# Optimization experiments

Measured on AMD Instinct MI355X. Metric: run time of the kernel, lower is better.

The kernel has to match this reference:

```python
import jax, jax.numpy as jnp
import numpy as np

N_NODES = 50000
N_EDGES = 800000
HIDDEN = 128
EDGE_DIM = 16
N_HEADS = 8
HEAD_DIM = HIDDEN // N_HEADS
SCALE = 1.0 / np.sqrt(HEAD_DIM).astype(np.float32)
LN_EPS = 1e-5


def setup_inputs() -> dict:
    key = jax.random.key(0)
    ks = jax.random.split(key, 24)
    s = 0.02

    def w(k, shape):
        return jax.random.normal(k, shape, dtype=jnp.float32) * s

    inp = {
        "node_features": jax.random.normal(ks[0], (N_NODES, HIDDEN), dtype=jnp.float32),
        "edge_index": jax.random.randint(ks[1], (2, N_EDGES), 0, N_NODES, dtype=jnp.int32),
        "edge_features": jax.random.normal(ks[2], (N_EDGES, EDGE_DIM), dtype=jnp.float32),
        # projections stored as [in, out] (y = x @ W + b)
        "Wq": w(ks[3], (HIDDEN, HIDDEN)), "bq": jnp.zeros((HIDDEN,), jnp.float32),
        "Wk": w(ks[4], (HIDDEN, HIDDEN)), "bk": jnp.zeros((HIDDEN,), jnp.float32),
        "Wv": w(ks[5], (HIDDEN, HIDDEN)), "bv": jnp.zeros((HIDDEN,), jnp.float32),
        "Wb1": w(ks[6], (EDGE_DIM, N_HEADS)), "bb1": jnp.zeros((N_HEADS,), jnp.float32),
        "Wb2": w(ks[7], (N_HEADS, N_HEADS)), "bb2": jnp.zeros((N_HEADS,), jnp.float32),
        "Wo": w(ks[8], (HIDDEN, HIDDEN)), "bo": jnp.zeros((HIDDEN,), jnp.float32),
        "Wf1": w(ks[9], (HIDDEN, 2 * HIDDEN)), "bf1": jnp.zeros((2 * HIDDEN,), jnp.float32),
        "Wf2": w(ks[10], (2 * HIDDEN, HIDDEN)), "bf2": jnp.zeros((HIDDEN,), jnp.float32),
        "g1": jnp.ones((HIDDEN,), jnp.float32), "be1": jnp.zeros((HIDDEN,), jnp.float32),
        "g2": jnp.ones((HIDDEN,), jnp.float32), "be2": jnp.zeros((HIDDEN,), jnp.float32),
    }
    return inp


def _layer_norm(x, gamma, beta):
    mu = jnp.mean(x, axis=-1, keepdims=True)
    var = jnp.mean(jnp.square(x - mu), axis=-1, keepdims=True)
    return (x - mu) * jax.lax.rsqrt(var + LN_EPS) * gamma + beta


def reference(node_features, edge_index, edge_features,
              Wq, bq, Wk, bk, Wv, bv, Wb1, bb1, Wb2, bb2,
              Wo, bo, Wf1, bf1, Wf2, bf2, g1, be1, g2, be2):
    n_nodes = node_features.shape[0]
    src, dst = edge_index[0], edge_index[1]

    q = (node_features @ Wq + bq).reshape(n_nodes, N_HEADS, HEAD_DIM)
    k = (node_features @ Wk + bk).reshape(n_nodes, N_HEADS, HEAD_DIM)
    v = (node_features @ Wv + bv).reshape(n_nodes, N_HEADS, HEAD_DIM)

    # per-edge attention logits [E, H]
    edge_bias = jax.nn.silu(edge_features @ Wb1 + bb1) @ Wb2 + bb2
    logits = jnp.sum(q[dst] * k[src], axis=-1) * SCALE + edge_bias

    # segment softmax over edges sharing the same dst node
    max_s = jax.ops.segment_max(logits, dst, num_segments=n_nodes)
    exp_s = jnp.exp(logits - max_s[dst])
    norm = jax.ops.segment_sum(exp_s, dst, num_segments=n_nodes)
    attn = exp_s / jnp.clip(norm[dst], 1e-12)

    # weighted aggregation [N, H, D] -> [N, hidden]
    weighted = attn[:, :, None] * v[src]
    aggregated = jax.ops.segment_sum(weighted, dst, num_segments=n_nodes)
    aggregated = aggregated.reshape(n_nodes, HIDDEN)

    x = _layer_norm(node_features + (aggregated @ Wo + bo), g1, be1)
    ffn = jax.nn.silu(x @ Wf1 + bf1) @ Wf2 + bf2
    return _layer_norm(x + ffn, g2, be2)
```

## Files before the change

kernel.cpp:

```cpp
#include <hip/hip_runtime.h>
#include <hip/hip_bf16.h>
#include <math.h>

#define HIDDEN 128
#define EDGE_DIM 16
#define N_HEADS 8
#define QK_SCALE 0.25f
#define LN_EPS 1e-5f

using bf16x8 = __attribute__((ext_vector_type(8))) short;
using f32x4 = __attribute__((ext_vector_type(4))) float;
using f32x4v = __attribute__((ext_vector_type(4))) float;
using f32x2 = __attribute__((ext_vector_type(2))) float;
using i32x4 = __attribute__((ext_vector_type(4))) int;
typedef __hip_bfloat16 bf16;

__device__ __forceinline__ float b2f(short u) {
  union { unsigned int i; float f; } c;
  c.i = ((unsigned int)(unsigned short)u) << 16;
  return c.f;
}
__device__ __forceinline__ short f2b(float f) {
  bf16 h = __float2bfloat16(f);
  union { bf16 b; short s; } c;
  c.b = h;
  return c.s;
}
__device__ __forceinline__ unsigned char f2fp8(float f) {
  int pk = __builtin_amdgcn_cvt_pk_fp8_f32(f, f, 0, false);
  return (unsigned char)(pk & 0xff);
}

__global__ __launch_bounds__(256) void conv_weights_kernel(
    const float* __restrict__ Wq, const float* __restrict__ Wk, const float* __restrict__ Wv,
    const float* __restrict__ bq, const float* __restrict__ bk, const float* __restrict__ bv,
    const float* __restrict__ Wo, const float* __restrict__ Wf1, const float* __restrict__ Wf2,
    bf16* __restrict__ Wqkv_t, bf16* __restrict__ Wo_t, bf16* __restrict__ Wf1_t,
    bf16* __restrict__ Wf2_t, float* __restrict__ bqkv) {
  int i = blockIdx.x * 256 + threadIdx.x;
  if (i < 49152) {
    int n = i >> 7, k = i & 127;
    const float* W = (n < 128) ? Wq : ((n < 256) ? Wk : Wv);
    int nn = n & 127;
    Wqkv_t[i] = __float2bfloat16(W[k * 128 + nn]);
  } else if (i < 65536) {
    int j = i - 49152;
    int n = j >> 7, k = j & 127;
    Wo_t[j] = __float2bfloat16(Wo[k * 128 + n]);
  } else if (i < 98304) {
    int j = i - 65536;
    int n = j >> 7, k = j & 127;
    Wf1_t[j] = __float2bfloat16(Wf1[k * 256 + n]);
  } else if (i < 131072) {
    int j = i - 98304;
    int n = j >> 8, k = j & 255;
    Wf2_t[j] = __float2bfloat16(Wf2[k * 128 + n]);
  }
  if (i < 384) bqkv[i] = (i < 128) ? bq[i] : ((i < 256) ? bk[i - 128] : bv[i - 256]);
}

template <int K, int EPI, int OUTBF, int AF32>
__global__ __launch_bounds__(256) void mfma_gemm_kernel(
    const void* __restrict__ Ap, const bf16* __restrict__ Wt,
    const float* __restrict__ bias, void* __restrict__ Cout, int M, int Nc) {
  const int tid = threadIdx.x;
  const int w = tid >> 6, l = tid & 63;
  const int wr = w >> 1, wc = w & 1;
  const int lr = l & 15, lk = l >> 4;
  const int bm = blockIdx.y * 64;
  const int bn = blockIdx.x * 128 + wc * 64;

  f32x4 acc[2][4] = {};
  const int arow0 = bm + wr * 32 + lr;

  for (int k0 = 0; k0 < K; k0 += 128) {
    bf16x8 bfr[4][4];
#pragma unroll
    for (int fn = 0; fn < 4; ++fn) {
      const bf16* wp = Wt + (size_t)(bn + fn * 16 + lr) * K + k0 + lk * 8;
#pragma unroll
      for (int ks = 0; ks < 4; ++ks) bfr[fn][ks] = *(const bf16x8*)(wp + ks * 32);
    }
    bf16x8 afr[2][4];
#pragma unroll
    for (int fr = 0; fr < 2; ++fr) {
      int row = arow0 + fr * 16;
      if (row >= M) row = M - 1;
      if (AF32) {
        const float* ap = (const float*)Ap + (size_t)row * K + k0 + lk * 8;
#pragma unroll
        for (int ks = 0; ks < 4; ++ks) {
          float4 x = *(const float4*)(ap + ks * 32);
          float4 y = *(const float4*)(ap + ks * 32 + 4);
          bf16x8 t;
          t[0] = f2b(x.x); t[1] = f2b(x.y); t[2] = f2b(x.z); t[3] = f2b(x.w);
          t[4] = f2b(y.x); t[5] = f2b(y.y); t[6] = f2b(y.z); t[7] = f2b(y.w);
          afr[fr][ks] = t;
        }
      } else {
        const bf16* ap = (const bf16*)Ap + (size_t)row * K + k0 + lk * 8;
#pragma unroll
        for (int ks = 0; ks < 4; ++ks) afr[fr][ks] = *(const bf16x8*)(ap + ks * 32);
      }
    }
#pragma unroll
    for (int ks = 0; ks < 4; ++ks)
#pragma unroll
      for (int fr = 0; fr < 2; ++fr)
#pragma unroll
        for (int fn = 0; fn < 4; ++fn)
          acc[fr][fn] = __builtin_amdgcn_mfma_f32_16x16x32_bf16(afr[fr][ks], bfr[fn][ks],
                                                                acc[fr][fn], 0, 0, 0);
  }

#pragma unroll
  for (int fn = 0; fn < 4; ++fn) {
    const int col = bn + fn * 16 + lr;
    const float bv = bias[col];
#pragma unroll
    for (int fr = 0; fr < 2; ++fr) {
      const int rbase = bm + wr * 32 + fr * 16 + lk * 4;
#pragma unroll
      for (int r = 0; r < 4; ++r) {
        int row = rbase + r;
        if (row < M) {
          float o = acc[fr][fn][r] + bv;
          if (EPI == 1) o = o / (1.f + __expf(-o));
          if (OUTBF)
            ((bf16*)Cout)[(size_t)row * Nc + col] = __float2bfloat16(o);
          else
            ((float*)Cout)[(size_t)row * Nc + col] = o;
        }
      }
    }
  }
}

__global__ __launch_bounds__(256) void mfma_gemm_qkv_kernel(
    const float* __restrict__ A, const bf16* __restrict__ Wt,
    const float* __restrict__ bias, bf16* __restrict__ qb,
    unsigned char* __restrict__ kv8, int M) {
  __shared__ __align__(16) char lds[64 * 272];
  const int tid = threadIdx.x;
  const int w = tid >> 6, l = tid & 63;
  const int wr = w >> 1, wc = w & 1;
  const int lr = l & 15, lk = l >> 4;
  const int bm = blockIdx.y * 64;
  const int bn = blockIdx.x * 128 + wc * 64;

  f32x4 acc[2][4] = {};
  const int arow0 = bm + wr * 32 + lr;

  {
    bf16x8 bfr[4][4];
#pragma unroll
    for (int fn = 0; fn < 4; ++fn) {
      const bf16* wp = Wt + (size_t)(bn + fn * 16 + lr) * 128 + lk * 8;
#pragma unroll
      for (int ks = 0; ks < 4; ++ks) bfr[fn][ks] = *(const bf16x8*)(wp + ks * 32);
    }
    bf16x8 afr[2][4];
#pragma unroll
    for (int fr = 0; fr < 2; ++fr) {
      int row = arow0 + fr * 16;
      if (row >= M) row = M - 1;
      const float* ap = A + (size_t)row * 128 + lk * 8;
#pragma unroll
      for (int ks = 0; ks < 4; ++ks) {
        float4 x = *(const float4*)(ap + ks * 32);
        float4 y = *(const float4*)(ap + ks * 32 + 4);
        bf16x8 t;
        t[0] = f2b(x.x); t[1] = f2b(x.y); t[2] = f2b(x.z); t[3] = f2b(x.w);
        t[4] = f2b(y.x); t[5] = f2b(y.y); t[6] = f2b(y.z); t[7] = f2b(y.w);
        afr[fr][ks] = t;
      }
    }
#pragma unroll
    for (int ks = 0; ks < 4; ++ks)
#pragma unroll
      for (int fr = 0; fr < 2; ++fr)
#pragma unroll
        for (int fn = 0; fn < 4; ++fn)
          acc[fr][fn] = __builtin_amdgcn_mfma_f32_16x16x32_bf16(afr[fr][ks], bfr[fn][ks],
                                                                acc[fr][fn], 0, 0, 0);
  }

  const bool isQ = (blockIdx.x == 0);
  if (isQ) {
    short* sq = (short*)lds;
#pragma unroll
    for (int fn = 0; fn < 4; ++fn) {
      const int col = wc * 64 + fn * 16 + lr;
      const float bv = bias[bn + fn * 16 + lr];
#pragma unroll
      for (int fr = 0; fr < 2; ++fr) {
#pragma unroll
        for (int r = 0; r < 4; ++r) {
          int rl = wr * 32 + fr * 16 + lk * 4 + r;
          sq[rl * 136 + col] = f2b(acc[fr][fn][r] + bv);
        }
      }
    }
  } else {
    unsigned char* s8 = (unsigned char*)lds;
#pragma unroll
    for (int fn = 0; fn < 4; ++fn) {
      const int col = wc * 64 + fn * 16 + lr;
      const float bv = bias[bn + fn * 16 + lr];
#pragma unroll
      for (int fr = 0; fr < 2; ++fr) {
#pragma unroll
        for (int r = 0; r < 4; ++r) {
          int rl = wr * 32 + fr * 16 + lk * 4 + r;
          s8[rl * 144 + col] = f2fp8(acc[fr][fn][r] + bv);
        }
      }
    }
  }
  __syncthreads();

  const int row = tid >> 2, seg = tid & 3;
  const int grow = bm + row;
  if (grow < M) {
    if (isQ) {
      const int4* src = (const int4*)(lds + row * 272 + seg * 64);
      int4* dst = (int4*)(qb + (size_t)grow * 128 + seg * 32);
      dst[0] = src[0];
      dst[1] = src[1];
      dst[2] = src[2];
      dst[3] = src[3];
    } else {
      const int4* src = (const int4*)(lds + row * 144 + seg * 32);
      int4* dst = (int4*)(kv8 + (size_t)grow * 256 + (blockIdx.x == 1 ? 0 : 128) + seg * 32);
      dst[0] = src[0];
      dst[1] = src[1];
    }
  }
}

template <int K>
__global__ __launch_bounds__(256) void mfma_gemm_ln_kernel(
    const bf16* __restrict__ A, const bf16* __restrict__ Wt,
    const float* __restrict__ bias, const float* __restrict__ R,
    const float* __restrict__ gam, const float* __restrict__ bet,
    float* __restrict__ y, bf16* __restrict__ yb, int M) {
  const int tid = threadIdx.x;
  const int w = tid >> 6, l = tid & 63;
  const int wr = w >> 1, wc = w & 1;
  const int lr = l & 15, lk = l >> 4;
  const int bm = blockIdx.x * 64;
  const int bn = wc * 64;

  f32x4 acc[2][4] = {};
  const int arow0 = bm + wr * 32 + lr;

  for (int k0 = 0; k0 < K; k0 += 128) {
    bf16x8 bfr[4][4];
#pragma unroll
    for (int fn = 0; fn < 4; ++fn) {
      const bf16* wp = Wt + (size_t)(bn + fn * 16 + lr) * K + k0 + lk * 8;
#pragma unroll
      for (int ks = 0; ks < 4; ++ks) bfr[fn][ks] = *(const bf16x8*)(wp + ks * 32);
    }
    bf16x8 afr[2][4];
#pragma unroll
    for (int fr = 0; fr < 2; ++fr) {
      int row = arow0 + fr * 16;
      if (row >= M) row = M - 1;
      const bf16* ap = A + (size_t)row * K + k0 + lk * 8;
#pragma unroll
      for (int ks = 0; ks < 4; ++ks) afr[fr][ks] = *(const bf16x8*)(ap + ks * 32);
    }
#pragma unroll
    for (int ks = 0; ks < 4; ++ks)
#pragma unroll
      for (int fr = 0; fr < 2; ++fr)
#pragma unroll
        for (int fn = 0; fn < 4; ++fn)
          acc[fr][fn] = __builtin_amdgcn_mfma_f32_16x16x32_bf16(afr[fr][ks], bfr[fn][ks],
                                                                acc[fr][fn], 0, 0, 0);
  }

  float bv[4], gv[4], ev[4];
#pragma unroll
  for (int fn = 0; fn < 4; ++fn) {
    int col = bn + fn * 16 + lr;
    bv[fn] = bias[col];
    gv[fn] = gam[col];
    ev[fn] = bet[col];
  }
  float ps[2][4], psq[2][4];
#pragma unroll
  for (int fr = 0; fr < 2; ++fr) {
#pragma unroll
    for (int r = 0; r < 4; ++r) {
      int row = bm + wr * 32 + fr * 16 + lk * 4 + r;
      int rrow = (row < M) ? row : (M - 1);
      float s = 0.f, sq = 0.f;
#pragma unroll
      for (int fn = 0; fn < 4; ++fn) {
        int col = bn + fn * 16 + lr;
        float o = acc[fr][fn][r] + bv[fn] + R[(size_t)rrow * HIDDEN + col];
        acc[fr][fn][r] = o;
        s += o;
        sq += o * o;
      }
      ps[fr][r] = s;
      psq[fr][r] = sq;
    }
  }
#pragma unroll
  for (int off = 1; off < 16; off <<= 1) {
#pragma unroll
    for (int fr = 0; fr < 2; ++fr)
#pragma unroll
      for (int r = 0; r < 4; ++r) {
        ps[fr][r] += __shfl_xor(ps[fr][r], off, 64);
        psq[fr][r] += __shfl_xor(psq[fr][r], off, 64);
      }
  }
  __shared__ float s_sum[2][64], s_sq[2][64];
  if (lr == 0) {
#pragma unroll
    for (int fr = 0; fr < 2; ++fr)
#pragma unroll
      for (int r = 0; r < 4; ++r) {
        int rl = wr * 32 + fr * 16 + lk * 4 + r;
        s_sum[wc][rl] = ps[fr][r];
        s_sq[wc][rl] = psq[fr][r];
      }
  }
  __syncthreads();
#pragma unroll
  for (int fr = 0; fr < 2; ++fr) {
#pragma unroll
    for (int r = 0; r < 4; ++r) {
      int rl = wr * 32 + fr * 16 + lk * 4 + r;
      int row = bm + rl;
      float tot = s_sum[0][rl] + s_sum[1][rl];
      float tsq = s_sq[0][rl] + s_sq[1][rl];
      float mean = tot * (1.f / 128.f);
      float var = tsq * (1.f / 128.f) - mean * mean;
      float rstd = rsqrtf(var + LN_EPS);
      if (row < M) {
#pragma unroll
        for (int fn = 0; fn < 4; ++fn) {
          int col = bn + fn * 16 + lr;
          float val = (acc[fr][fn][r] - mean) * rstd * gv[fn] + ev[fn];
          if (y) y[(size_t)row * HIDDEN + col] = val;
          if (yb) yb[(size_t)row * HIDDEN + col] = __float2bfloat16(val);
        }
      }
    }
  }
}

__global__ void hist_kernel(const int* __restrict__ dst, int* __restrict__ counts, int E) {
  int e = blockIdx.x * blockDim.x + threadIdx.x;
  if (e < E) atomicAdd(&counts[dst[e]], 1);
}

__device__ __forceinline__ int wave_incl_scan(int x, int lane) {
  int incl = x;
#pragma unroll
  for (int off = 1; off < 64; off <<= 1) {
    int y = __shfl_up(incl, off, 64);
    if (lane >= off) incl += y;
  }
  return incl;
}

__global__ __launch_bounds__(256) void scan_block_kernel(const int* __restrict__ counts,
                                                         int* __restrict__ offs,
                                                         int* __restrict__ btot, int N) {
  __shared__ int s4[4];
  int tid = threadIdx.x;
  int i = blockIdx.x * 256 + tid;
  int lane = tid & 63, wv = tid >> 6;
  int x = (i < N) ? counts[i] : 0;
  int incl = wave_incl_scan(x, lane);
  if (lane == 63) s4[wv] = incl;
  __syncthreads();
  if (tid == 0) {
    int s = 0;
#pragma unroll
    for (int j = 0; j < 4; ++j) { int t = s4[j]; s4[j] = s; s += t; }
    btot[blockIdx.x] = s;
  }
  __syncthreads();
  if (i < N) offs[i] = s4[wv] + incl - x;
}

__global__ __launch_bounds__(256) void scan_tot_kernel(int* __restrict__ btot, int nb) {
  __shared__ int s4[4];
  __shared__ int carry;
  int tid = threadIdx.x;
  int lane = tid & 63, wv = tid >> 6;
  if (tid == 0) carry = 0;
  __syncthreads();
  for (int c0 = 0; c0 < nb; c0 += 256) {
    int i = c0 + tid;
    int x = (i < nb) ? btot[i] : 0;
    int incl = wave_incl_scan(x, lane);
    if (lane == 63) s4[wv] = incl;
    __syncthreads();
    if (tid == 0) {
      int s = 0;
#pragma unroll
      for (int j = 0; j < 4; ++j) { int t = s4[j]; s4[j] = s; s += t; }
    }
    __syncthreads();
    int base = carry + s4[wv];
    if (i < nb) btot[i] = base + incl - x;
    __syncthreads();
    if (tid == 255) carry = base + incl;
    __syncthreads();
  }
}

__global__ __launch_bounds__(256) void scan_add_kernel(int* __restrict__ offs,
                                                       const int* __restrict__ btot,
                                                       int N, int E) {
  int i = blockIdx.x * 256 + threadIdx.x;
  if (i < N) offs[i] += btot[blockIdx.x];
  if (i == 0) offs[N] = E;
}

__global__ __launch_bounds__(256) void scatter_mlp_kernel(
    const int* __restrict__ dst, const float* __restrict__ ef,
    const float* __restrict__ Wb1, const float* __restrict__ bb1,
    const float* __restrict__ Wb2, const float* __restrict__ bb2,
    const int* __restrict__ offs, int* __restrict__ cursor,
    int* __restrict__ eid_csr, bf16* __restrict__ eb, int E) {
  __shared__ float w1[128], w2[64], b1[8], b2[8];
  int tid = threadIdx.x;
  if (tid < 128) w1[tid] = Wb1[tid];
  else if (tid < 192) w2[tid - 128] = Wb2[tid - 128];
  else if (tid < 200) b1[tid - 192] = bb1[tid - 192];
  else if (tid < 208) b2[tid - 200] = bb2[tid - 200];
  __syncthreads();

  int e = blockIdx.x * 256 + tid;
  if (e >= E) return;

  const f32x4v* p4 = (const f32x4v*)(ef + (size_t)e * 16);
  f32x4v f0 = __builtin_nontemporal_load(p4 + 0);
  f32x4v f1 = __builtin_nontemporal_load(p4 + 1);
  f32x4v f2 = __builtin_nontemporal_load(p4 + 2);
  f32x4v f3 = __builtin_nontemporal_load(p4 + 3);
  float x[16] = {f0[0], f0[1], f0[2], f0[3], f1[0], f1[1], f1[2], f1[3],
                 f2[0], f2[1], f2[2], f2[3], f3[0], f3[1], f3[2], f3[3]};

  float h[8];
#pragma unroll
  for (int j = 0; j < 8; ++j) h[j] = b1[j];
#pragma unroll
  for (int i = 0; i < 16; ++i) {
    float xi = x[i];
#pragma unroll
    for (int j = 0; j < 8; ++j) h[j] = fmaf(xi, w1[i * 8 + j], h[j]);
  }
#pragma unroll
  for (int j = 0; j < 8; ++j) h[j] = h[j] / (1.f + __expf(-h[j]));

  float o[8];
#pragma unroll
  for (int j = 0; j < 8; ++j) o[j] = b2[j];
#pragma unroll
  for (int jj = 0; jj < 8; ++jj) {
    float hj = h[jj];
#pragma unroll
    for (int j = 0; j < 8; ++j) o[j] = fmaf(hj, w2[jj * 8 + j], o[j]);
  }
  bf16x8 o8;
#pragma unroll
  for (int j = 0; j < 8; ++j) o8[j] = f2b(o[j]);
  __builtin_nontemporal_store(o8, (bf16x8*)(eb + (size_t)e * 8));

  int d = dst[e];
  int p = offs[d] + atomicAdd(&cursor[d], 1);
  __builtin_nontemporal_store(e, eid_csr + p);
}

__global__ __launch_bounds__(256) void node_attn_kernel(
    const bf16* __restrict__ qb, const unsigned char* __restrict__ kv8,
    const int* __restrict__ eid_csr, const int* __restrict__ srcA,
    const bf16* __restrict__ eb, const int* __restrict__ offs,
    bf16* __restrict__ agg, int Nn) {
  int n = blockIdx.x * 4 + (threadIdx.x >> 6);
  if (n >= Nn) return;
  int l = threadIdx.x & 63;
  int g = l >> 3;
  int il = l & 7;

  int s0 = offs[n], s1 = offs[n + 1];
  bf16* orow = agg + (size_t)n * HIDDEN + il * 16;
  if (s0 >= s1) {
    if (g == 0) {
      bf16x8 z = {};
      *(bf16x8*)(orow) = z;
      *(bf16x8*)(orow + 8) = z;
    }
    return;
  }

  const bf16* qrow = qb + (size_t)n * 128 + il * 16;
  bf16x8 qa = *(const bf16x8*)(qrow);
  bf16x8 qb8 = *(const bf16x8*)(qrow + 8);
  float qf[16];
#pragma unroll
  for (int j = 0; j < 8; ++j) {
    qf[j] = b2f(qa[j]) * QK_SCALE;
    qf[8 + j] = b2f(qb8[j]) * QK_SCALE;
  }

  float lsum = 0.f;
  float acc[16] = {};

  int p = s0 + g;
  int pc = (p < s1) ? p : s1 - 1;
  int eid = eid_csr[pc];
  int s = srcA[eid];

  for (int p0 = s0; p0 < s1; p0 += 8) {
    bool valid = (p0 + g) < s1;
    int ce = eid, cs = s;
    int pn = p0 + 8 + g;
    if (pn < s1) {
      eid = eid_csr[pn];
      s = srcA[eid];
    }
    float ebv = b2f(eb[(size_t)ce * 8 + il]);
    const unsigned char* kvrow = kv8 + (size_t)cs * 256 + il * 16;
    i32x4 kw = *(const i32x4*)(kvrow);
    i32x4 vw = *(const i32x4*)(kvrow + 128);

    float prod = 0.f;
#pragma unroll
    for (int w2 = 0; w2 < 4; ++w2) {
      f32x2 lo = __builtin_amdgcn_cvt_pk_f32_fp8(kw[w2], false);
      f32x2 hi = __builtin_amdgcn_cvt_pk_f32_fp8(kw[w2], true);
      prod = fmaf(qf[w2 * 4 + 0], lo[0], prod);
      prod = fmaf(qf[w2 * 4 + 1], lo[1], prod);
      prod = fmaf(qf[w2 * 4 + 2], hi[0], prod);
      prod = fmaf(qf[w2 * 4 + 3], hi[1], prod);
    }
    float pe = valid ? __expf(prod + ebv) : 0.f;
    lsum += pe;
#pragma unroll
    for (int w2 = 0; w2 < 4; ++w2) {
      f32x2 lo = __builtin_amdgcn_cvt_pk_f32_fp8(vw[w2], false);
      f32x2 hi = __builtin_amdgcn_cvt_pk_f32_fp8(vw[w2], true);
      acc[w2 * 4 + 0] = fmaf(pe, lo[0], acc[w2 * 4 + 0]);
      acc[w2 * 4 + 1] = fmaf(pe, lo[1], acc[w2 * 4 + 1]);
      acc[w2 * 4 + 2] = fmaf(pe, hi[0], acc[w2 * 4 + 2]);
      acc[w2 * 4 + 3] = fmaf(pe, hi[1], acc[w2 * 4 + 3]);
    }
  }

#pragma unroll
  for (int off = 8; off < 64; off <<= 1) {
    lsum += __shfl_xor(lsum, off, 64);
#pragma unroll
    for (int j = 0; j < 16; ++j) acc[j] += __shfl_xor(acc[j], off, 64);
  }

  if (g == 0) {
    float inv = (lsum > 0.f) ? 1.f / lsum : 0.f;
    bf16x8 o0, o1;
#pragma unroll
    for (int j = 0; j < 8; ++j) {
      o0[j] = f2b(acc[j] * inv);
      o1[j] = f2b(acc[8 + j] * inv);
    }
    *(bf16x8*)(orow) = o0;
    *(bf16x8*)(orow + 8) = o1;
  }
}

extern "C" void kernel_launch(void* const* d_in, const int* in_sizes, int n_in,
                              void* d_out, int out_size, void* d_ws, size_t ws_size,
                              hipStream_t stream) {
  const float* nf = (const float*)d_in[0];
  const int* ei = (const int*)d_in[1];
  const float* ef = (const float*)d_in[2];
  const float* Wq = (const float*)d_in[3];
  const float* bq = (const float*)d_in[4];
  const float* Wk = (const float*)d_in[5];
  const float* bk_ = (const float*)d_in[6];
  const float* Wv = (const float*)d_in[7];
  const float* bv = (const float*)d_in[8];
  const float* Wb1 = (const float*)d_in[9];
  const float* bb1 = (const float*)d_in[10];
  const float* Wb2 = (const float*)d_in[11];
  const float* bb2 = (const float*)d_in[12];
  const float* Wo = (const float*)d_in[13];
  const float* bo = (const float*)d_in[14];
  const float* Wf1 = (const float*)d_in[15];
  const float* bf1 = (const float*)d_in[16];
  const float* Wf2 = (const float*)d_in[17];
  const float* bf2 = (const float*)d_in[18];
  const float* g1 = (const float*)d_in[19];
  const float* be1 = (const float*)d_in[20];
  const float* g2 = (const float*)d_in[21];
  const float* be2 = (const float*)d_in[22];

  const int N = in_sizes[0] / HIDDEN;
  const int E = in_sizes[2] / EDGE_DIM;
  const int* srcA = ei;
  const int* dstA = ei + E;

  char* base = (char*)d_ws;
  size_t off = 0;
  auto alloc = [&](size_t bytes) {
    off = (off + 255) & ~(size_t)255;
    char* p = base + off;
    off += bytes;
    return p;
  };

  size_t qb_bytes = (size_t)N * 128 * 2;
  size_t kv_bytes = (size_t)N * 256;
  size_t hb_bytes = (size_t)N * 256 * 2;
  char* regB = alloc(hb_bytes > qb_bytes + kv_bytes ? hb_bytes : qb_bytes + kv_bytes);
  bf16* qb = (bf16*)regB;
  unsigned char* kv8 = (unsigned char*)(regB + qb_bytes);
  bf16* hbuf = (bf16*)regB;
  bf16* agg = (bf16*)alloc((size_t)N * HIDDEN * 2);
  float* x1 = (float*)alloc((size_t)N * HIDDEN * 4);
  bf16* x1b = (bf16*)alloc((size_t)N * HIDDEN * 2);
  int* eid_csr = (int*)alloc((size_t)E * 4);
  bf16* eb = (bf16*)alloc((size_t)E * N_HEADS * 2);
  int* counts = (int*)alloc((size_t)N * 8);
  int* cursor = counts + N;
  int* offs = (int*)alloc((size_t)(N + 1) * 4);
  const int nb = (N + 255) / 256;
  int* btot = (int*)alloc((size_t)nb * 4);
  bf16* Wqkv_t = (bf16*)alloc(384 * 128 * 2);
  bf16* Wo_t = (bf16*)alloc(128 * 128 * 2);
  bf16* Wf1_t = (bf16*)alloc(256 * 128 * 2);
  bf16* Wf2_t = (bf16*)alloc(128 * 256 * 2);
  float* bqkv = (float*)alloc(384 * 4);

  float* outp = (float*)d_out;
  const int mb64 = (N + 63) / 64;
  const int eblocks = (E + 255) / 256;

  conv_weights_kernel<<<512, 256, 0, stream>>>(Wq, Wk, Wv, bq, bk_, bv, Wo, Wf1, Wf2,
                                               Wqkv_t, Wo_t, Wf1_t, Wf2_t, bqkv);

  mfma_gemm_qkv_kernel<<<dim3(3, mb64), 256, 0, stream>>>(nf, Wqkv_t, bqkv, qb, kv8, N);

  hipMemsetAsync(counts, 0, (size_t)N * 8, stream);
  hist_kernel<<<eblocks, 256, 0, stream>>>(dstA, counts, E);
  scan_block_kernel<<<nb, 256, 0, stream>>>(counts, offs, btot, N);
  scan_tot_kernel<<<1, 256, 0, stream>>>(btot, nb);
  scan_add_kernel<<<nb, 256, 0, stream>>>(offs, btot, N, E);
  scatter_mlp_kernel<<<eblocks, 256, 0, stream>>>(dstA, ef, Wb1, bb1, Wb2, bb2,
                                                  offs, cursor, eid_csr, eb, E);

  node_attn_kernel<<<(N + 3) / 4, 256, 0, stream>>>(qb, kv8, eid_csr, srcA, eb, offs,
                                                    agg, N);

  mfma_gemm_ln_kernel<128><<<mb64, 256, 0, stream>>>(agg, Wo_t, bo, nf, g1, be1, x1, x1b, N);

  mfma_gemm_kernel<128, 1, 1, 0><<<dim3(2, mb64), 256, 0, stream>>>(
      x1b, Wf1_t, bf1, hbuf, N, 256);

  mfma_gemm_ln_kernel<256><<<mb64, 256, 0, stream>>>(hbuf, Wf2_t, bf2, x1, g2, be2,
                                                     outp, nullptr, N);
}
```

Baseline: 282.6 us.

## Pack src index and fp8 edge bias into CSR-ordered 16-byte edge records

```diff
diff --git a/kernel.cpp b/kernel.cpp
--- a/kernel.cpp
+++ b/kernel.cpp
@@ -7,6 +7,8 @@
 #define N_HEADS 8
 #define QK_SCALE 0.25f
 #define LN_EPS 1e-5f
+#define EB_SCALE 256.0f
+#define EB_INV (1.0f / 256.0f)
 
 using bf16x8 = __attribute__((ext_vector_type(8))) short;
 using f32x4 = __attribute__((ext_vector_type(4))) float;
@@ -427,11 +429,11 @@
 }
 
 __global__ __launch_bounds__(256) void scatter_mlp_kernel(
-    const int* __restrict__ dst, const float* __restrict__ ef,
-    const float* __restrict__ Wb1, const float* __restrict__ bb1,
-    const float* __restrict__ Wb2, const float* __restrict__ bb2,
-    const int* __restrict__ offs, int* __restrict__ cursor,
-    int* __restrict__ eid_csr, bf16* __restrict__ eb, int E) {
+    const int* __restrict__ dst, const int* __restrict__ src,
+    const float* __restrict__ ef, const float* __restrict__ Wb1,
+    const float* __restrict__ bb1, const float* __restrict__ Wb2,
+    const float* __restrict__ bb2, const int* __restrict__ offs,
+    int* __restrict__ cursor, i32x4* __restrict__ es16, int E) {
   __shared__ float w1[128], w2[64], b1[8], b2[8];
   int tid = threadIdx.x;
   if (tid < 128) w1[tid] = Wb1[tid];
@@ -472,20 +474,22 @@
 #pragma unroll
     for (int j = 0; j < 8; ++j) o[j] = fmaf(hj, w2[jj * 8 + j], o[j]);
   }
-  bf16x8 o8;
-#pragma unroll
-  for (int j = 0; j < 8; ++j) o8[j] = f2b(o[j]);
-  __builtin_nontemporal_store(o8, (bf16x8*)(eb + (size_t)e * 8));
+
+  int lo = __builtin_amdgcn_cvt_pk_fp8_f32(o[0] * EB_SCALE, o[1] * EB_SCALE, 0, false);
+  lo = __builtin_amdgcn_cvt_pk_fp8_f32(o[2] * EB_SCALE, o[3] * EB_SCALE, lo, true);
+  int hi = __builtin_amdgcn_cvt_pk_fp8_f32(o[4] * EB_SCALE, o[5] * EB_SCALE, 0, false);
+  hi = __builtin_amdgcn_cvt_pk_fp8_f32(o[6] * EB_SCALE, o[7] * EB_SCALE, hi, true);
 
   int d = dst[e];
   int p = offs[d] + atomicAdd(&cursor[d], 1);
-  __builtin_nontemporal_store(e, eid_csr + p);
+  i32x4 rec;
+  rec[0] = src[e]; rec[1] = lo; rec[2] = hi; rec[3] = 0;
+  __builtin_nontemporal_store(rec, es16 + p);
 }
 
 __global__ __launch_bounds__(256) void node_attn_kernel(
     const bf16* __restrict__ qb, const unsigned char* __restrict__ kv8,
-    const int* __restrict__ eid_csr, const int* __restrict__ srcA,
-    const bf16* __restrict__ eb, const int* __restrict__ offs,
+    const i32x4* __restrict__ es16, const int* __restrict__ offs,
     bf16* __restrict__ agg, int Nn) {
   int n = blockIdx.x * 4 + (threadIdx.x >> 6);
   if (n >= Nn) return;
@@ -516,21 +520,18 @@
 
   float lsum = 0.f;
   float acc[16] = {};
-
-  int p = s0 + g;
-  int pc = (p < s1) ? p : s1 - 1;
-  int eid = eid_csr[pc];
-  int s = srcA[eid];
+  const int ebshift = (il & 2) << 3;
 
   for (int p0 = s0; p0 < s1; p0 += 8) {
-    bool valid = (p0 + g) < s1;
-    int ce = eid, cs = s;
-    int pn = p0 + 8 + g;
-    if (pn < s1) {
-      eid = eid_csr[pn];
-      s = srcA[eid];
-    }
-    float ebv = b2f(eb[(size_t)ce * 8 + il]);
+    int p = p0 + g;
+    bool valid = p < s1;
+    int pc = valid ? p : s1 - 1;
+    i32x4 rec = es16[pc];
+    int cs = rec[0];
+    unsigned ebw = (unsigned)((il < 4) ? rec[1] : rec[2]);
+    f32x2 ebp = __builtin_amdgcn_cvt_pk_f32_fp8(ebw >> ebshift, false);
+    float ebv = ((il & 1) ? ebp[1] : ebp[0]) * EB_INV;
+
     const unsigned char* kvrow = kv8 + (size_t)cs * 256 + il * 16;
     i32x4 kw = *(const i32x4*)(kvrow);
     i32x4 vw = *(const i32x4*)(kvrow + 128);
@@ -629,8 +630,7 @@
   bf16* agg = (bf16*)alloc((size_t)N * HIDDEN * 2);
   float* x1 = (float*)alloc((size_t)N * HIDDEN * 4);
   bf16* x1b = (bf16*)alloc((size_t)N * HIDDEN * 2);
-  int* eid_csr = (int*)alloc((size_t)E * 4);
-  bf16* eb = (bf16*)alloc((size_t)E * N_HEADS * 2);
+  i32x4* es16 = (i32x4*)alloc((size_t)E * 16);
   int* counts = (int*)alloc((size_t)N * 8);
   int* cursor = counts + N;
   int* offs = (int*)alloc((size_t)(N + 1) * 4);
@@ -656,11 +656,10 @@
   scan_block_kernel<<<nb, 256, 0, stream>>>(counts, offs, btot, N);
   scan_tot_kernel<<<1, 256, 0, stream>>>(btot, nb);
   scan_add_kernel<<<nb, 256, 0, stream>>>(offs, btot, N, E);
-  scatter_mlp_kernel<<<eblocks, 256, 0, stream>>>(dstA, ef, Wb1, bb1, Wb2, bb2,
-                                                  offs, cursor, eid_csr, eb, E);
-
-  node_attn_kernel<<<(N + 3) / 4, 256, 0, stream>>>(qb, kv8, eid_csr, srcA, eb, offs,
-                                                    agg, N);
+  scatter_mlp_kernel<<<eblocks, 256, 0, stream>>>(dstA, srcA, ef, Wb1, bb1, Wb2, bb2,
+                                                  offs, cursor, es16, E);
+
+  node_attn_kernel<<<(N + 3) / 4, 256, 0, stream>>>(qb, kv8, es16, offs, agg, N);
 
   mfma_gemm_ln_kernel<128><<<mb64, 256, 0, stream>>>(agg, Wo_t, bo, nf, g1, be1, x1, x1b, N);
 
```

New measurement: 272.2 us. 3.7% less time.
